# Kernel optimization log

Measured on AMD Instinct MI355X. Metric: run time of the kernel, lower is better.

## Reference

```python
import jax, jax.numpy as jnp
import numpy as np

IGNORE = 5
N_CLASS = 5
MAX_VIEWS = 2048
MAX_VIEWS_BG = 4096


def setup_inputs() -> dict:
    key = jax.random.key(0)
    ks = jax.random.split(key, 8)
    B, C, H, W = 8, 512, 128, 128
    HF, WF = 1024, 1024
    feats = jax.random.normal(ks[0], (B, C, H, W), dtype=jnp.float32)
    labels = jax.random.uniform(ks[1], (B, HF, WF, N_CLASS), dtype=jnp.float32)
    predicts = jax.random.randint(ks[2], (B, H, W), 0, N_CLASS).astype(jnp.int32)
    s = 0.02
    w1 = jax.random.normal(ks[3], (512, 512), jnp.float32) * s
    b1 = jnp.zeros((512,), jnp.float32)
    w2 = jax.random.normal(ks[4], (256, 512), jnp.float32) * s
    b2 = jnp.zeros((256,), jnp.float32)
    w3 = jax.random.normal(ks[5], (256, 256), jnp.float32) * s
    b3 = jnp.zeros((256,), jnp.float32)
    return dict(feats=feats, labels=labels, predicts=predicts,
                w1=w1, b1=b1, w2=w2, b2=b2, w3=w3, b3=b3)


def _leaky(x):
    return jnp.where(x >= 0, x, 0.2 * x)


def _proj_head(x, w1, b1, w2, b2, w3, b3):
    # Linear -> LeakyReLU(0.2) -> Linear -> LeakyReLU(0.2) -> Linear, then L2-normalize (dim=1)
    h = _leaky(x @ w1.T + b1)
    h = _leaky(h @ w2.T + b2)
    h = h @ w3.T + b3
    nrm = jnp.maximum(jnp.linalg.norm(h, axis=1, keepdims=True), 1e-12)
    return h / nrm


def _sample_class(y_hat, y, feats0, c, mv):
    """Stratified hard/easy pixel selection for class c, padded to static size mv.
    Deterministic take-first-k replaces torch.randperm for reproducibility."""
    N = y_hat.shape[0]
    hard = (y_hat == c) & (y != c)
    easy = (y_hat == c) & (y == c)
    nh = hard.sum().astype(jnp.int32)
    ne = easy.sum().astype(jnp.int32)
    cnt = nh + ne
    valid = (cnt > 1).astype(jnp.int32)   # classes with <=1 pixel are skipped in the original
    n_sel = jnp.minimum(cnt, mv) * valid
    both = (2 * nh >= n_sel) & (2 * ne >= n_sel)
    hk = jnp.where(both, n_sel // 2,
                   jnp.where(2 * nh >= n_sel, n_sel - ne, nh))
    ek = n_sel - hk
    idx = jnp.arange(N, dtype=jnp.int32)
    hsel = hard & ((jnp.cumsum(hard) - 1) < hk)   # first hk hard pixels
    esel = easy & ((jnp.cumsum(easy) - 1) < ek)   # first ek easy pixels
    # stream-compaction: hard first, then easy, then padding
    sort_key = jnp.where(hsel, idx, jnp.where(esel, idx + N, 2 * N))
    order = jnp.argsort(sort_key)[:mv]            # static slice of size mv
    row_ok = jnp.arange(mv) < n_sel
    X = feats0[order] * row_ok[:, None]           # zero-pad invalid rows
    yc = jnp.where(row_ok, c, IGNORE)
    return X, yc.astype(jnp.int32)


def reference(feats, labels, predicts, w1, b1, w2, b2, w3, b3):
    B, C, H, W = feats.shape
    lab = jnp.argmax(labels, axis=-1)             # [B, HF, WF]
    sh, sw = lab.shape[1] // H, lab.shape[2] // W
    lab_ds = lab[:, ::sh, ::sw]                   # nearest-neighbor downsample (integer factor)
    # original _hard_anchor_sampling returns inside the batch loop -> only image 0 contributes
    y_hat = lab_ds[0].reshape(-1).astype(jnp.int32)
    y = predicts[0].reshape(-1).astype(jnp.int32)
    feats0 = feats[0].transpose(1, 2, 0).reshape(H * W, C)  # NHWC flatten
    Xs, ys = [], []
    for c in range(N_CLASS):                      # static small class loop
        mv = MAX_VIEWS_BG if c == 0 else MAX_VIEWS
        Xc, yc = _sample_class(y_hat, y, feats0, c, mv)
        Xs.append(Xc)
        ys.append(yc)
    X_ = jnp.concatenate(Xs, axis=0)              # [MV_bg + 4*MV, 512]
    y_ = jnp.concatenate(ys, axis=0)
    anchors = _proj_head(X_, w1, b1, w2, b2, w3, b3)
    return anchors, y_
```

## Files before the change

kernel.cpp:

```cpp
#include <hip/hip_runtime.h>

#define HW 16384
#define IGN 5
#define ROWS_TOTAL 12288
#define ANCH_ELEMS (ROWS_TOTAL * 256)

typedef __bf16 bf16x8 __attribute__((ext_vector_type(8)));
typedef float f32x4 __attribute__((ext_vector_type(4)));
typedef unsigned long long ull;

#define GLDS16(g, l)                                                                     \
    __builtin_amdgcn_global_load_lds((__attribute__((address_space(1))) const void*)(g), \
                                     (__attribute__((address_space(3))) void*)(l), 16, 0, 0)

__global__ void prep_kernel(const float* __restrict__ labels, const int* __restrict__ predicts,
                            int* __restrict__ y_hat, ull* __restrict__ maskH,
                            ull* __restrict__ maskE) {
    int p = blockIdx.x * 256 + threadIdx.x;
    int pr = p >> 7, pc = p & 127;
    const float* lp = labels + ((size_t)(pr * 8) * 1024 + (size_t)(pc * 8)) * 5;
    float best = lp[0];
    int bi = 0;
#pragma unroll
    for (int c = 1; c < 5; ++c) {
        float v = lp[c];
        if (v > best) { best = v; bi = c; }
    }
    y_hat[p] = bi;
    int yy = predicts[p];
    int chunk = p >> 6;
    int lane = threadIdx.x & 63;
#pragma unroll
    for (int c = 0; c < 5; ++c) {
        ull mh = __ballot(bi == c && yy != c);
        ull me = __ballot(bi == c && yy == c);
        if (lane == 0) {
            maskH[c * 256 + chunk] = mh;
            maskE[c * 256 + chunk] = me;
        }
    }
}

__global__ void scan_kernel(const ull* __restrict__ maskH, const ull* __restrict__ maskE,
                            int* __restrict__ baseH, int* __restrict__ baseE,
                            int* __restrict__ nsel, int* __restrict__ hkA,
                            int* __restrict__ ekA) {
    int c = threadIdx.x >> 6;
    int lane = threadIdx.x & 63;
    if (c >= 5) return;
    int ph[4], pe[4];
    int sh = 0, se = 0;
#pragma unroll
    for (int k = 0; k < 4; ++k) {
        int ch = lane * 4 + k;
        ph[k] = sh;
        sh += __popcll(maskH[c * 256 + ch]);
        pe[k] = se;
        se += __popcll(maskE[c * 256 + ch]);
    }
    int incH = sh, incE = se;
#pragma unroll
    for (int d = 1; d < 64; d <<= 1) {
        int t = __shfl_up(incH, d);
        if (lane >= d) incH += t;
        t = __shfl_up(incE, d);
        if (lane >= d) incE += t;
    }
    int exH = incH - sh, exE = incE - se;
#pragma unroll
    for (int k = 0; k < 4; ++k) {
        baseH[c * 256 + lane * 4 + k] = exH + ph[k];
        baseE[c * 256 + lane * 4 + k] = exE + pe[k];
    }
    int nh = __shfl(incH, 63), ne = __shfl(incE, 63);
    if (lane == 0) {
        int mv = (c == 0) ? 4096 : 2048;
        int cnt = nh + ne;
        int n_sel = (cnt > 1) ? ((cnt < mv) ? cnt : mv) : 0;
        int hk;
        if ((2 * nh >= n_sel) && (2 * ne >= n_sel)) hk = n_sel >> 1;
        else if (2 * nh >= n_sel) hk = n_sel - ne;
        else hk = nh;
        nsel[c] = n_sel;
        hkA[c] = hk;
        ekA[c] = n_sel - hk;
    }
}

__global__ void write_inv_kernel(const int* __restrict__ y_hat, const int* __restrict__ predicts,
                                 const ull* __restrict__ maskH, const ull* __restrict__ maskE,
                                 const int* __restrict__ baseH, const int* __restrict__ baseE,
                                 const int* __restrict__ hkA, const int* __restrict__ ekA,
                                 int* __restrict__ inv) {
    int p = blockIdx.x * 256 + threadIdx.x;
    int chunk = p >> 6;
    int lane = threadIdx.x & 63;
    int c = y_hat[p];
    ull mh = maskH[c * 256 + chunk];
    ull me = maskE[c * 256 + chunk];
    ull below = (1ull << lane) - 1ull;
    int cls_base = (c == 0) ? 0 : 4096 + (c - 1) * 2048;
    int res = -1;
    if ((mh >> lane) & 1ull) {
        int pos = baseH[c * 256 + chunk] + __popcll(mh & below);
        if (pos < hkA[c]) res = cls_base + pos;
    } else if ((me >> lane) & 1ull) {
        int pos = baseE[c * 256 + chunk] + __popcll(me & below);
        if (pos < ekA[c]) res = cls_base + hkA[c] + pos;
    }
    inv[p] = res;
}

__global__ void conv_x_kernel(const float* __restrict__ F, __bf16* __restrict__ Xb) {
    __shared__ float t[32 * 33];
    int pb = blockIdx.x * 32, chb = blockIdx.y * 32;
    int tid = threadIdx.x;
    int il = tid & 31;
    int grp = tid >> 5;
#pragma unroll
    for (int it = 0; it < 4; ++it) {
        int ch = grp + it * 8;
        t[il * 33 + ch] = F[(size_t)(chb + ch) * HW + pb + il];
    }
    __syncthreads();
#pragma unroll
    for (int it = 0; it < 4; ++it) {
        int p = grp + it * 8;
        Xb[(size_t)(pb + p) * 512 + chb + il] = (__bf16)t[p * 33 + il];
    }
}

__global__ void conv_w_kernel(const float* __restrict__ w1, const float* __restrict__ w2,
                              const float* __restrict__ w3, __bf16* __restrict__ w1b,
                              __bf16* __restrict__ w2b, __bf16* __restrict__ w3b) {
    int i = blockIdx.x * 256 + threadIdx.x;
    if (i < 262144) w1b[i] = (__bf16)w1[i];
    else if (i < 393216) w2b[i - 262144] = (__bf16)w2[i - 262144];
    else if (i < 458752) w3b[i - 393216] = (__bf16)w3[i - 393216];
}

__global__ void fill_out_kernel(float* __restrict__ out, const int* __restrict__ nsel) {
    int idx = blockIdx.x * 256 + threadIdx.x;
    if (idx < ANCH_ELEMS / 4) {
        ((float4*)out)[idx] = make_float4(0.f, 0.f, 0.f, 0.f);
    } else {
        int r = idx - ANCH_ELEMS / 4;
        if (r < ROWS_TOTAL) {
            int c, rin;
            if (r < 4096) { c = 0; rin = r; }
            else { c = 1 + ((r - 4096) >> 11); rin = (r - 4096) & 2047; }
            out[ANCH_ELEMS + r] = (float)(rin < nsel[c] ? c : IGN);
        }
    }
}

__global__ __launch_bounds__(256) void gemm_bt(const __bf16* __restrict__ A,
                                               const __bf16* __restrict__ Bw,
                                               const float* __restrict__ bias,
                                               __bf16* __restrict__ C, int M, int N, int K,
                                               int leaky) {
    const int BK = 32;
    __shared__ __bf16 As[128 * 32];
    __shared__ __bf16 Bs[128 * 32];
    int tid = threadIdx.x;
    int lane = tid & 63;
    int wave_base = tid & 0xC0;
    int wave = tid >> 6;
    int wm = (wave >> 1) * 64, wn = (wave & 1) * 64;
    int mb = blockIdx.y * 128, nb = blockIdx.x * 128;
    int l15 = lane & 15, quad = lane >> 4;

    f32x4 acc[4][4] = {};

    for (int kt = 0; kt < K; kt += BK) {
#pragma unroll
        for (int r = 0; r < 2; ++r) {
            int cc = tid + r * 256;
            int row = cc >> 2, ko = (cc & 3) * 8;
            GLDS16(A + (size_t)(mb + row) * K + kt + ko,
                   As + (size_t)(r * 256 + wave_base) * 8);
            GLDS16(Bw + (size_t)(nb + row) * K + kt + ko,
                   Bs + (size_t)(r * 256 + wave_base) * 8);
        }
        __syncthreads();
        bf16x8 af[4], bq[4];
#pragma unroll
        for (int i = 0; i < 4; ++i)
            af[i] = *(const bf16x8*)(As + (wm + i * 16 + l15) * BK + quad * 8);
#pragma unroll
        for (int j = 0; j < 4; ++j)
            bq[j] = *(const bf16x8*)(Bs + (wn + j * 16 + l15) * BK + quad * 8);
#pragma unroll
        for (int i = 0; i < 4; ++i)
#pragma unroll
            for (int j = 0; j < 4; ++j)
                acc[i][j] = __builtin_amdgcn_mfma_f32_16x16x32_bf16(af[i], bq[j], acc[i][j], 0, 0, 0);
        __syncthreads();
    }

#pragma unroll
    for (int i = 0; i < 4; ++i) {
#pragma unroll
        for (int j = 0; j < 4; ++j) {
            int col = nb + wn + j * 16 + l15;
            float bv = bias[col];
#pragma unroll
            for (int r = 0; r < 4; ++r) {
                int row = mb + wm + i * 16 + quad * 4 + r;
                float v = acc[i][j][r] + bv;
                if (leaky) v = (v >= 0.f) ? v : 0.2f * v;
                C[(size_t)row * N + col] = (__bf16)v;
            }
        }
    }
}

__global__ __launch_bounds__(256) void gemm3_norm_scatter(const __bf16* __restrict__ A,
                                                          const __bf16* __restrict__ W,
                                                          const float* __restrict__ bias,
                                                          const int* __restrict__ inv,
                                                          float* __restrict__ out) {
    const int BK = 32, K = 256;
    __shared__ __bf16 As[64 * 32];
    __shared__ __bf16 Bs[256 * 32];
    __shared__ __bf16 lo[64 * 264];
    __shared__ float nrm[64];
    int tid = threadIdx.x;
    int lane = tid & 63, wave = tid >> 6;
    int wave_base = tid & 0xC0;
    int l15 = lane & 15, quad = lane >> 4;
    int mb = blockIdx.x * 64;
    int wn = wave * 64;

    if (tid < 64) nrm[tid] = 0.f;

    f32x4 acc[4][4] = {};

    for (int kt = 0; kt < K; kt += BK) {
        {
            int row = tid >> 2, ko = (tid & 3) * 8;
            GLDS16(A + (size_t)(mb + row) * K + kt + ko, As + (size_t)wave_base * 8);
        }
#pragma unroll
        for (int r = 0; r < 4; ++r) {
            int cc = tid + r * 256;
            int row = cc >> 2, ko = (cc & 3) * 8;
            GLDS16(W + (size_t)row * K + kt + ko, Bs + (size_t)(r * 256 + wave_base) * 8);
        }
        __syncthreads();
        bf16x8 af[4], bq[4];
#pragma unroll
        for (int i = 0; i < 4; ++i)
            af[i] = *(const bf16x8*)(As + (i * 16 + l15) * BK + quad * 8);
#pragma unroll
        for (int j = 0; j < 4; ++j)
            bq[j] = *(const bf16x8*)(Bs + (wn + j * 16 + l15) * BK + quad * 8);
#pragma unroll
        for (int i = 0; i < 4; ++i)
#pragma unroll
            for (int j = 0; j < 4; ++j)
                acc[i][j] = __builtin_amdgcn_mfma_f32_16x16x32_bf16(af[i], bq[j], acc[i][j], 0, 0, 0);
        __syncthreads();
    }

#pragma unroll
    for (int i = 0; i < 4; ++i) {
#pragma unroll
        for (int r = 0; r < 4; ++r) {
            int row = i * 16 + quad * 4 + r;
            float s = 0.f;
#pragma unroll
            for (int j = 0; j < 4; ++j) {
                int col = wn + j * 16 + l15;
                float v = acc[i][j][r] + bias[col];
                lo[row * 264 + col] = (__bf16)v;
                s += v * v;
            }
            atomicAdd(&nrm[row], s);
        }
    }
    __syncthreads();
    if (tid < 64) nrm[tid] = 1.0f / fmaxf(sqrtf(nrm[tid]), 1e-12f);
    __syncthreads();

    for (int r = 0; r < 64; ++r) {
        int orow = inv[mb + r];
        if (orow >= 0) out[(size_t)orow * 256 + tid] = (float)lo[r * 264 + tid] * nrm[r];
    }
}

extern "C" void kernel_launch(void* const* d_in, const int* in_sizes, int n_in,
                              void* d_out, int out_size, void* d_ws, size_t ws_size,
                              hipStream_t stream) {
    const float* feats = (const float*)d_in[0];
    const float* labels = (const float*)d_in[1];
    const int* predicts = (const int*)d_in[2];
    const float* w1 = (const float*)d_in[3];
    const float* b1 = (const float*)d_in[4];
    const float* w2 = (const float*)d_in[5];
    const float* b2 = (const float*)d_in[6];
    const float* w3 = (const float*)d_in[7];
    const float* b3 = (const float*)d_in[8];
    float* out = (float*)d_out;
    char* ws = (char*)d_ws;

    int* y_hat = (int*)(ws + 0);
    int* inv = (int*)(ws + (64 << 10));
    int* nsel = (int*)(ws + (128 << 10));
    int* hkA = (int*)(ws + (128 << 10) + 64);
    int* ekA = (int*)(ws + (128 << 10) + 128);
    ull* maskH = (ull*)(ws + (136 << 10));
    ull* maskE = (ull*)(ws + (148 << 10));
    int* baseH = (int*)(ws + (160 << 10));
    int* baseE = (int*)(ws + (168 << 10));
    __bf16* w1b = (__bf16*)(ws + (256 << 10));
    __bf16* w2b = (__bf16*)(ws + (768 << 10));
    __bf16* w3b = (__bf16*)(ws + (1024 << 10));
    __bf16* Xb = (__bf16*)(ws + (2ull << 20));
    __bf16* H1 = (__bf16*)(ws + (18ull << 20));
    __bf16* H2 = (__bf16*)(ws + (34ull << 20));

    prep_kernel<<<64, 256, 0, stream>>>(labels, predicts, y_hat, maskH, maskE);
    scan_kernel<<<1, 320, 0, stream>>>(maskH, maskE, baseH, baseE, nsel, hkA, ekA);
    write_inv_kernel<<<64, 256, 0, stream>>>(y_hat, predicts, maskH, maskE, baseH, baseE,
                                             hkA, ekA, inv);
    conv_x_kernel<<<dim3(512, 16), 256, 0, stream>>>(feats, Xb);
    conv_w_kernel<<<1792, 256, 0, stream>>>(w1, w2, w3, w1b, w2b, w3b);
    fill_out_kernel<<<3120, 256, 0, stream>>>(out, nsel);
    gemm_bt<<<dim3(4, 128), 256, 0, stream>>>(Xb, w1b, b1, H1, HW, 512, 512, 1);
    gemm_bt<<<dim3(2, 128), 256, 0, stream>>>(H1, w2b, b2, H2, HW, 256, 512, 1);
    gemm3_norm_scatter<<<256, 256, 0, stream>>>(H2, w3b, b3, inv, out);
}
```

Baseline: 447.7 us.

## Gather selected rows before projection GEMMs and swizzle LDS tiles with BK=64

Replaces the inverse map with a forward map from output rows to pixels. The projection head now runs only on the 12288 selected rows, gathered in the first GEMM, instead of on all 16384 pixels. The last GEMM writes every output row densely and zeroes padding rows through the norm factor, which removes the separate zero-fill kernel and the scattered writes. The GEMMs also move to K-tiles of 64 with an XOR-swizzled LDS layout to avoid bank conflicts, and the first two use 64-row M tiles. The risk is that padding rows gather pixel 0 and depend on the zero scale being applied.

```diff
diff --git a/kernel.cpp b/kernel.cpp
--- a/kernel.cpp
+++ b/kernel.cpp
@@ -13,9 +13,13 @@
     __builtin_amdgcn_global_load_lds((__attribute__((address_space(1))) const void*)(g), \
                                      (__attribute__((address_space(3))) void*)(l), 16, 0, 0)
 
+__device__ __forceinline__ int swz_off(int row, int chunk) {
+    return row * 64 + ((chunk ^ (row & 7)) * 8);
+}
+
 __global__ void prep_kernel(const float* __restrict__ labels, const int* __restrict__ predicts,
                             int* __restrict__ y_hat, ull* __restrict__ maskH,
-                            ull* __restrict__ maskE) {
+                            ull* __restrict__ maskE, int* __restrict__ fwd) {
     int p = blockIdx.x * 256 + threadIdx.x;
     int pr = p >> 7, pc = p & 127;
     const float* lp = labels + ((size_t)(pr * 8) * 1024 + (size_t)(pc * 8)) * 5;
@@ -27,6 +31,7 @@
         if (v > best) { best = v; bi = c; }
     }
     y_hat[p] = bi;
+    if (p < ROWS_TOTAL) fwd[p] = -1;
     int yy = predicts[p];
     int chunk = p >> 6;
     int lane = threadIdx.x & 63;
@@ -87,11 +92,12 @@
     }
 }
 
-__global__ void write_inv_kernel(const int* __restrict__ y_hat, const int* __restrict__ predicts,
+__global__ void write_inv_kernel(const int* __restrict__ y_hat,
                                  const ull* __restrict__ maskH, const ull* __restrict__ maskE,
                                  const int* __restrict__ baseH, const int* __restrict__ baseE,
                                  const int* __restrict__ hkA, const int* __restrict__ ekA,
-                                 int* __restrict__ inv) {
+                                 const int* __restrict__ nsel, int* __restrict__ fwd,
+                                 float* __restrict__ out) {
     int p = blockIdx.x * 256 + threadIdx.x;
     int chunk = p >> 6;
     int lane = threadIdx.x & 63;
@@ -108,7 +114,13 @@
         int pos = baseE[c * 256 + chunk] + __popcll(me & below);
         if (pos < ekA[c]) res = cls_base + hkA[c] + pos;
     }
-    inv[p] = res;
+    if (res >= 0) fwd[res] = p;
+    if (p < ROWS_TOTAL) {
+        int cc, rin;
+        if (p < 4096) { cc = 0; rin = p; }
+        else { cc = 1 + ((p - 4096) >> 11); rin = (p - 4096) & 2047; }
+        out[ANCH_ELEMS + p] = (float)(rin < nsel[cc] ? cc : IGN);
+    }
 }
 
 __global__ void conv_x_kernel(const float* __restrict__ F, __bf16* __restrict__ Xb) {
@@ -139,67 +151,71 @@
     else if (i < 458752) w3b[i - 393216] = (__bf16)w3[i - 393216];
 }
 
-__global__ void fill_out_kernel(float* __restrict__ out, const int* __restrict__ nsel) {
-    int idx = blockIdx.x * 256 + threadIdx.x;
-    if (idx < ANCH_ELEMS / 4) {
-        ((float4*)out)[idx] = make_float4(0.f, 0.f, 0.f, 0.f);
-    } else {
-        int r = idx - ANCH_ELEMS / 4;
-        if (r < ROWS_TOTAL) {
-            int c, rin;
-            if (r < 4096) { c = 0; rin = r; }
-            else { c = 1 + ((r - 4096) >> 11); rin = (r - 4096) & 2047; }
-            out[ANCH_ELEMS + r] = (float)(rin < nsel[c] ? c : IGN);
-        }
-    }
-}
-
 __global__ __launch_bounds__(256) void gemm_bt(const __bf16* __restrict__ A,
+                                               const int* __restrict__ fwd,
                                                const __bf16* __restrict__ Bw,
                                                const float* __restrict__ bias,
-                                               __bf16* __restrict__ C, int M, int N, int K,
+                                               __bf16* __restrict__ C, int N, int K,
                                                int leaky) {
-    const int BK = 32;
-    __shared__ __bf16 As[128 * 32];
-    __shared__ __bf16 Bs[128 * 32];
+    const int BK = 64;
+    __shared__ __bf16 As[64 * 64];
+    __shared__ __bf16 Bs[128 * 64];
     int tid = threadIdx.x;
     int lane = tid & 63;
     int wave_base = tid & 0xC0;
     int wave = tid >> 6;
-    int wm = (wave >> 1) * 64, wn = (wave & 1) * 64;
-    int mb = blockIdx.y * 128, nb = blockIdx.x * 128;
+    int wm = (wave >> 1) * 32, wn = (wave & 1) * 64;
+    int mb = blockIdx.y * 64, nb = blockIdx.x * 128;
     int l15 = lane & 15, quad = lane >> 4;
 
-    f32x4 acc[4][4] = {};
+    const __bf16* srcA[2];
+    const __bf16* srcB[4];
+#pragma unroll
+    for (int r = 0; r < 2; ++r) {
+        int cc = tid + r * 256;
+        int row = cc >> 3, ch = cc & 7;
+        int g = mb + row;
+        int pix = fwd ? fwd[g] : g;
+        if (pix < 0) pix = 0;
+        srcA[r] = A + (size_t)pix * K + ((ch ^ (row & 7)) * 8);
+    }
+#pragma unroll
+    for (int r = 0; r < 4; ++r) {
+        int cc = tid + r * 256;
+        int row = cc >> 3, ch = cc & 7;
+        srcB[r] = Bw + (size_t)(nb + row) * K + ((ch ^ (row & 7)) * 8);
+    }
+
+    f32x4 acc[2][4] = {};
 
     for (int kt = 0; kt < K; kt += BK) {
 #pragma unroll
-        for (int r = 0; r < 2; ++r) {
-            int cc = tid + r * 256;
-            int row = cc >> 2, ko = (cc & 3) * 8;
-            GLDS16(A + (size_t)(mb + row) * K + kt + ko,
-                   As + (size_t)(r * 256 + wave_base) * 8);
-            GLDS16(Bw + (size_t)(nb + row) * K + kt + ko,
-                   Bs + (size_t)(r * 256 + wave_base) * 8);
-        }
+        for (int r = 0; r < 2; ++r)
+            GLDS16(srcA[r] + kt, As + (size_t)(r * 256 + wave_base) * 8);
+#pragma unroll
+        for (int r = 0; r < 4; ++r)
+            GLDS16(srcB[r] + kt, Bs + (size_t)(r * 256 + wave_base) * 8);
         __syncthreads();
-        bf16x8 af[4], bq[4];
-#pragma unroll
-        for (int i = 0; i < 4; ++i)
-            af[i] = *(const bf16x8*)(As + (wm + i * 16 + l15) * BK + quad * 8);
-#pragma unroll
-        for (int j = 0; j < 4; ++j)
-            bq[j] = *(const bf16x8*)(Bs + (wn + j * 16 + l15) * BK + quad * 8);
-#pragma unroll
-        for (int i = 0; i < 4; ++i)
+#pragma unroll
+        for (int kk = 0; kk < 2; ++kk) {
+            bf16x8 af[2], bq[4];
+#pragma unroll
+            for (int i = 0; i < 2; ++i)
+                af[i] = *(const bf16x8*)(As + swz_off(wm + i * 16 + l15, quad + kk * 4));
 #pragma unroll
             for (int j = 0; j < 4; ++j)
-                acc[i][j] = __builtin_amdgcn_mfma_f32_16x16x32_bf16(af[i], bq[j], acc[i][j], 0, 0, 0);
+                bq[j] = *(const bf16x8*)(Bs + swz_off(wn + j * 16 + l15, quad + kk * 4));
+#pragma unroll
+            for (int i = 0; i < 2; ++i)
+#pragma unroll
+                for (int j = 0; j < 4; ++j)
+                    acc[i][j] = __builtin_amdgcn_mfma_f32_16x16x32_bf16(af[i], bq[j], acc[i][j], 0, 0, 0);
+        }
         __syncthreads();
     }
 
 #pragma unroll
-    for (int i = 0; i < 4; ++i) {
+    for (int i = 0; i < 2; ++i) {
 #pragma unroll
         for (int j = 0; j < 4; ++j) {
             int col = nb + wn + j * 16 + l15;
@@ -215,14 +231,14 @@
     }
 }
 
-__global__ __launch_bounds__(256) void gemm3_norm_scatter(const __bf16* __restrict__ A,
-                                                          const __bf16* __restrict__ W,
-                                                          const float* __restrict__ bias,
-                                                          const int* __restrict__ inv,
-                                                          float* __restrict__ out) {
-    const int BK = 32, K = 256;
-    __shared__ __bf16 As[64 * 32];
-    __shared__ __bf16 Bs[256 * 32];
+__global__ __launch_bounds__(256) void gemm3_norm(const __bf16* __restrict__ A,
+                                                  const __bf16* __restrict__ W,
+                                                  const float* __restrict__ bias,
+                                                  const int* __restrict__ fwd,
+                                                  float* __restrict__ out) {
+    const int BK = 64, K = 256;
+    __shared__ __bf16 As[64 * 64];
+    __shared__ __bf16 Bs[256 * 64];
     __shared__ __bf16 lo[64 * 264];
     __shared__ float nrm[64];
     int tid = threadIdx.x;
@@ -234,32 +250,46 @@
 
     if (tid < 64) nrm[tid] = 0.f;
 
+    const __bf16* srcA[2];
+    const __bf16* srcB[8];
+#pragma unroll
+    for (int r = 0; r < 2; ++r) {
+        int cc = tid + r * 256;
+        int row = cc >> 3, ch = cc & 7;
+        srcA[r] = A + (size_t)(mb + row) * K + ((ch ^ (row & 7)) * 8);
+    }
+#pragma unroll
+    for (int r = 0; r < 8; ++r) {
+        int cc = tid + r * 256;
+        int row = cc >> 3, ch = cc & 7;
+        srcB[r] = W + (size_t)row * K + ((ch ^ (row & 7)) * 8);
+    }
+
     f32x4 acc[4][4] = {};
 
     for (int kt = 0; kt < K; kt += BK) {
-        {
-            int row = tid >> 2, ko = (tid & 3) * 8;
-            GLDS16(A + (size_t)(mb + row) * K + kt + ko, As + (size_t)wave_base * 8);
-        }
-#pragma unroll
-        for (int r = 0; r < 4; ++r) {
-            int cc = tid + r * 256;
-            int row = cc >> 2, ko = (cc & 3) * 8;
-            GLDS16(W + (size_t)row * K + kt + ko, Bs + (size_t)(r * 256 + wave_base) * 8);
-        }
+#pragma unroll
+        for (int r = 0; r < 2; ++r)
+            GLDS16(srcA[r] + kt, As + (size_t)(r * 256 + wave_base) * 8);
+#pragma unroll
+        for (int r = 0; r < 8; ++r)
+            GLDS16(srcB[r] + kt, Bs + (size_t)(r * 256 + wave_base) * 8);
         __syncthreads();
-        bf16x8 af[4], bq[4];
-#pragma unroll
-        for (int i = 0; i < 4; ++i)
-            af[i] = *(const bf16x8*)(As + (i * 16 + l15) * BK + quad * 8);
-#pragma unroll
-        for (int j = 0; j < 4; ++j)
-            bq[j] = *(const bf16x8*)(Bs + (wn + j * 16 + l15) * BK + quad * 8);
-#pragma unroll
-        for (int i = 0; i < 4; ++i)
+#pragma unroll
+        for (int kk = 0; kk < 2; ++kk) {
+            bf16x8 af[4], bq[4];
+#pragma unroll
+            for (int i = 0; i < 4; ++i)
+                af[i] = *(const bf16x8*)(As + swz_off(i * 16 + l15, quad + kk * 4));
 #pragma unroll
             for (int j = 0; j < 4; ++j)
-                acc[i][j] = __builtin_amdgcn_mfma_f32_16x16x32_bf16(af[i], bq[j], acc[i][j], 0, 0, 0);
+                bq[j] = *(const bf16x8*)(Bs + swz_off(wn + j * 16 + l15, quad + kk * 4));
+#pragma unroll
+            for (int i = 0; i < 4; ++i)
+#pragma unroll
+                for (int j = 0; j < 4; ++j)
+                    acc[i][j] = __builtin_amdgcn_mfma_f32_16x16x32_bf16(af[i], bq[j], acc[i][j], 0, 0, 0);
+        }
         __syncthreads();
     }
 
@@ -280,12 +310,15 @@
         }
     }
     __syncthreads();
-    if (tid < 64) nrm[tid] = 1.0f / fmaxf(sqrtf(nrm[tid]), 1e-12f);
+    if (tid < 64) {
+        float f = 1.0f / fmaxf(sqrtf(nrm[tid]), 1e-12f);
+        nrm[tid] = (fwd[mb + tid] >= 0) ? f : 0.f;
+    }
     __syncthreads();
 
+#pragma unroll 4
     for (int r = 0; r < 64; ++r) {
-        int orow = inv[mb + r];
-        if (orow >= 0) out[(size_t)orow * 256 + tid] = (float)lo[r * 264 + tid] * nrm[r];
+        out[(size_t)(mb + r) * 256 + tid] = (float)lo[r * 264 + tid] * nrm[r];
     }
 }
 
@@ -305,7 +338,7 @@
     char* ws = (char*)d_ws;
 
     int* y_hat = (int*)(ws + 0);
-    int* inv = (int*)(ws + (64 << 10));
+    int* fwd = (int*)(ws + (64 << 10));
     int* nsel = (int*)(ws + (128 << 10));
     int* hkA = (int*)(ws + (128 << 10) + 64);
     int* ekA = (int*)(ws + (128 << 10) + 128);
@@ -320,14 +353,13 @@
     __bf16* H1 = (__bf16*)(ws + (18ull << 20));
     __bf16* H2 = (__bf16*)(ws + (34ull << 20));
 
-    prep_kernel<<<64, 256, 0, stream>>>(labels, predicts, y_hat, maskH, maskE);
+    prep_kernel<<<64, 256, 0, stream>>>(labels, predicts, y_hat, maskH, maskE, fwd);
     scan_kernel<<<1, 320, 0, stream>>>(maskH, maskE, baseH, baseE, nsel, hkA, ekA);
-    write_inv_kernel<<<64, 256, 0, stream>>>(y_hat, predicts, maskH, maskE, baseH, baseE,
-                                             hkA, ekA, inv);
+    write_inv_kernel<<<64, 256, 0, stream>>>(y_hat, maskH, maskE, baseH, baseE, hkA, ekA,
+                                             nsel, fwd, out);
     conv_x_kernel<<<dim3(512, 16), 256, 0, stream>>>(feats, Xb);
     conv_w_kernel<<<1792, 256, 0, stream>>>(w1, w2, w3, w1b, w2b, w3b);
-    fill_out_kernel<<<3120, 256, 0, stream>>>(out, nsel);
-    gemm_bt<<<dim3(4, 128), 256, 0, stream>>>(Xb, w1b, b1, H1, HW, 512, 512, 1);
-    gemm_bt<<<dim3(2, 128), 256, 0, stream>>>(H1, w2b, b2, H2, HW, 256, 512, 1);
-    gemm3_norm_scatter<<<256, 256, 0, stream>>>(H2, w3b, b3, inv, out);
-}
+    gemm_bt<<<dim3(4, 192), 256, 0, stream>>>(Xb, fwd, w1b, b1, H1, 512, 512, 1);
+    gemm_bt<<<dim3(2, 192), 256, 0, stream>>>(H1, nullptr, w2b, b2, H2, 256, 512, 1);
+    gemm3_norm<<<192, 256, 0, stream>>>(H2, w3b, b3, fwd, out);
+}
```

New measurement: 428.8 us. -4.2%, faster.
